# Kernel tuning notes

Measured on AMD Instinct MI355X. Metric: run time of the kernel, lower is better.

## Reference

```python
import jax, jax.numpy as jnp
import numpy as np

B, N, C = 2, 6, 64
D_BINS, D_MIN, D_MAX = 64, 1.0, 60.0
IMG_H, IMG_W = 256, 704
FH, FW = 16, 44  # image_size / 16
BEV_H, BEV_W = 200, 200
XR = (-50.0, 50.0)
YR = (-50.0, 50.0)
BN_EPS = 1e-5


def create_frustum():
    # (D, FH, FW, 3) with last dim = (x_pix, y_pix, depth)
    ds = jnp.linspace(D_MIN, D_MAX, D_BINS)
    xs = jnp.linspace(0.0, IMG_W - 1.0, FW)
    ys = jnp.linspace(0.0, IMG_H - 1.0, FH)
    d, y, x = jnp.meshgrid(ds, ys, xs, indexing='ij')
    return jnp.stack([x, y, d], axis=-1)


def _conv(x, w, b, pad):
    y = jax.lax.conv_general_dilated(x, w, (1, 1), [(pad, pad), (pad, pad)],
                                     dimension_numbers=('NCHW', 'OIHW', 'NCHW'))
    return y + b[None, :, None, None]


def setup_inputs():
    key = jax.random.key(0)
    ks = jax.random.split(key, 4)
    features = jax.random.normal(ks[0], (B, N, C, FH, FW), jnp.float32)
    # realistic pinhole intrinsics
    fx = fy = 500.0
    K = jnp.array([[fx, 0.0, IMG_W / 2.0], [0.0, fy, IMG_H / 2.0], [0.0, 0.0, 1.0]], jnp.float32)
    intrinsics = jnp.broadcast_to(K, (B, N, 3, 3)).astype(jnp.float32)
    # cam2ego: yaw rotation per camera + small translation
    yaws = jnp.arange(N, dtype=jnp.float32) * (2.0 * np.pi / N)
    def ext(yaw):
        c, s = jnp.cos(yaw), jnp.sin(yaw)
        R = jnp.array([[c, -s, 0.0], [s, c, 0.0], [0.0, 0.0, 1.0]])
        return jnp.eye(4).at[:3, :3].set(R).at[:3, 3].set(jnp.array([1.0, 0.0, 1.5]))
    extrinsics = jnp.broadcast_to(jax.vmap(ext)(yaws), (B, N, 4, 4)).astype(jnp.float32)
    # DepthNet params: conv3x3(C->C) -> BN -> ReLU -> conv1x1(C->D)
    w1 = jax.random.normal(ks[1], (C, C, 3, 3), jnp.float32) * 0.05
    b1 = jnp.zeros((C,), jnp.float32)
    gamma = jnp.ones((C,), jnp.float32)
    beta = jnp.zeros((C,), jnp.float32)
    rmean = jnp.zeros((C,), jnp.float32)
    rvar = jnp.ones((C,), jnp.float32)
    w2 = jax.random.normal(ks[2], (D_BINS, C, 1, 1), jnp.float32) * 0.05
    b2 = jnp.zeros((D_BINS,), jnp.float32)
    return dict(features=features, intrinsics=intrinsics, extrinsics=extrinsics,
                w1=w1, b1=b1, gamma=gamma, beta=beta, rmean=rmean, rvar=rvar, w2=w2, b2=b2)


def reference(features, intrinsics, extrinsics, w1, b1, gamma, beta, rmean, rvar, w2, b2):
    feat = features.reshape(B * N, C, FH, FW)
    # DepthNet (BN in eval mode with running stats)
    h = _conv(feat, w1, b1, 1)
    h = (h - rmean[None, :, None, None]) * (gamma / jnp.sqrt(rvar + BN_EPS))[None, :, None, None] \
        + beta[None, :, None, None]
    h = jax.nn.relu(h)
    depth_logits = _conv(h, w2, b2, 0)                 # (BN, D, FH, FW)
    depth_probs = jax.nn.softmax(depth_logits, axis=1)
    # lift: outer product of features and depth distribution
    vol = feat[:, :, None] * depth_probs[:, None]      # (BN, C, D, FH, FW)
    vol = vol.reshape(B, N, C, D_BINS, FH, FW)

    frustum = create_frustum()                         # (D, FH, FW, 3)
    x, y, d = frustum[..., 0], frustum[..., 1], frustum[..., 2]
    pts = jnp.stack([x * d, y * d, d], axis=0).reshape(3, -1)   # (3, P), P = D*FH*FW
    Kinv = jnp.linalg.inv(intrinsics)                  # (B, N, 3, 3)
    cam = jnp.einsum('bnij,jp->bnip', Kinv, pts)       # camera-frame points
    R, t = extrinsics[..., :3, :3], extrinsics[..., :3, 3]
    ego = jnp.einsum('bnij,bnjp->bnip', R, cam) + t[..., None]  # (B, N, 3, P)

    resx = (XR[1] - XR[0]) / BEV_W
    resy = (YR[1] - YR[0]) / BEV_H
    ix = jnp.floor((ego[:, :, 0] - XR[0]) / resx).astype(jnp.int32)  # (B, N, P)
    iy = jnp.floor((ego[:, :, 1] - YR[0]) / resy).astype(jnp.int32)
    valid = (ix >= 0) & (ix < BEV_W) & (iy >= 0) & (iy < BEV_H)
    bidx = jnp.arange(B, dtype=jnp.int32)[:, None, None]
    idx = jnp.where(valid, bidx * (BEV_H * BEV_W) + iy * BEV_W + ix, 0)

    # splat: scatter-add depth-weighted features into the BEV grid
    vol_pts = vol.reshape(B, N, C, -1) * valid[:, :, None].astype(vol.dtype)
    vals = vol_pts.transpose(0, 1, 3, 2).reshape(-1, C)  # (B*N*P, C)
    bev = jax.ops.segment_sum(vals, idx.reshape(-1), num_segments=B * BEV_H * BEV_W)
    return bev.reshape(B, BEV_H, BEV_W, C).transpose(0, 3, 1, 2)  # (B, C, bevH, bevW)
```

## Files before the change

### kernel.cpp

```cpp
#include <hip/hip_runtime.h>
#include <math.h>

#define B_   2
#define N_   6
#define C_   64
#define D_   64
#define FH_  16
#define FW_  44
#define BN_  (B_*N_)
#define PIX_ (FH_*FW_)
#define NPIX (BN_*PIX_)
#define NPTS (BN_*D_*PIX_)
#define PPBN (D_*PIX_)
#define BEVH 200
#define BEVW 200
#define NCELL (BEVH*BEVW)
#define NBCELL (B_*NCELL)
#define NSCANB ((NBCELL + 255)/256)
#define PPW  32
#define GBLK (NPTS/(PPW*4))
#define NXCD 8
#define GCHUNK (GBLK/NXCD)
#define SCBLK (NPTS/256)

#define NB_ZOUT 5000
#define NB_ZSP  313
#define NB_TW   160
#define NB_PREP 1
#define NB_FT   132
#define NB_SETUP (NB_ZOUT + NB_ZSP + NB_TW + NB_PREP + NB_FT)

__global__ __launch_bounds__(256) void setup_kernel(
        const float* __restrict__ feat, const float* __restrict__ w1,
        const float* __restrict__ w2,
        const float* __restrict__ gamma, const float* __restrict__ beta,
        const float* __restrict__ rmean, const float* __restrict__ rvar,
        const float* __restrict__ intr,
        float* __restrict__ zt, int* __restrict__ startp,
        float* __restrict__ w1t, float* __restrict__ w2t,
        float* __restrict__ bns, float* __restrict__ bnsh,
        float* __restrict__ kinv, float* __restrict__ feat_t) {
#pragma clang fp contract(off)
    __shared__ float lds[64][65];
    int blk = blockIdx.x;
    int t   = threadIdx.x;

    if (blk < NB_ZOUT) {
        ((float4*)zt)[blk*256 + t] = float4{0.f, 0.f, 0.f, 0.f};
        return;
    }
    blk -= NB_ZOUT;
    if (blk < NB_ZSP) {
        int i = blk*256 + t;
        if (i < NBCELL + 1) startp[i] = 0;
        return;
    }
    blk -= NB_ZSP;
    if (blk < NB_TW) {
        int idx = blk*256 + t;
        if (idx < C_*C_*9) {
            int cout  = idx / (C_*9);
            int r     = idx % (C_*9);
            int cin   = r / 9;
            int tap   = r % 9;
            int chunk = cin >> 4;
            int g4    = (cin & 15) >> 2;
            int l4    = cin & 3;
            w1t[((((chunk*9 + tap)*4 + g4)*64 + cout)*4) + l4] = w1[idx];
        } else if (idx < C_*C_*9 + D_*C_) {
            int j = idx - C_*C_*9;
            int d = j / C_, c = j % C_;
            w2t[c*D_ + d] = w2[j];
        }
        return;
    }
    blk -= NB_TW;
    if (blk < NB_PREP) {
        if (t < C_) {
            float s = gamma[t] / sqrtf(rvar[t] + 1e-5f);
            bns[t]  = s;
            bnsh[t] = beta[t] - rmean[t] * s;
        }
        if (t < BN_) {
            const float* K = intr + t*9;
            float A[3][3];
            for (int r = 0; r < 3; r++)
                for (int cc = 0; cc < 3; cc++) A[r][cc] = K[r*3 + cc];
            int ipiv[3];
            for (int j = 0; j < 3; j++) {
                int p = j; float mx = fabsf(A[j][j]);
                for (int i = j+1; i < 3; i++) {
                    float v = fabsf(A[i][j]);
                    if (v > mx) { mx = v; p = i; }
                }
                ipiv[j] = p;
                if (p != j)
                    for (int k = 0; k < 3; k++) { float tm = A[j][k]; A[j][k] = A[p][k]; A[p][k] = tm; }
                float rpiv = 1.0f / A[j][j];
                for (int i = j+1; i < 3; i++) A[i][j] = A[i][j] * rpiv;
                for (int k = j+1; k < 3; k++)
                    for (int i = j+1; i < 3; i++)
                        A[i][k] = A[i][k] - A[i][j] * A[j][k];
            }
            for (int j = 0; j < 3; j++) {
                float ajj = 1.0f / A[j][j];
                A[j][j] = ajj;
                float najj = -ajj;
                for (int jj = 0; jj < j; jj++) {
                    float temp = A[jj][j];
                    for (int i = 0; i < jj; i++) A[i][j] = A[i][j] + temp * A[i][jj];
                    A[jj][j] = A[jj][j] * A[jj][jj];
                }
                for (int i = 0; i < j; i++) A[i][j] = A[i][j] * najj;
            }
            for (int j = 1; j >= 0; j--) {
                float work[3];
                for (int i = j+1; i < 3; i++) { work[i] = A[i][j]; A[i][j] = 0.0f; }
                for (int k = j+1; k < 3; k++)
                    for (int i = 0; i < 3; i++)
                        A[i][j] = A[i][j] - A[i][k] * work[k];
            }
            for (int j = 2; j >= 0; j--) {
                int p = ipiv[j];
                if (p != j)
                    for (int i = 0; i < 3; i++) { float tm = A[i][j]; A[i][j] = A[i][p]; A[i][p] = tm; }
            }
            for (int k = 0; k < 9; k++) kinv[t*9 + k] = A[k/3][k%3];
        }
        return;
    }
    blk -= NB_PREP;
    {
        int bn   = blk / 11;
        int pb   = (blk % 11) * 64;
        int lane = t & 63;
        int r0   = t >> 6;
#pragma unroll
        for (int rr = 0; rr < 16; rr++) {
            int c = r0 + 4*rr;
            lds[c][lane] = feat[((size_t)bn*C_ + c)*PIX_ + pb + lane];
        }
        __syncthreads();
#pragma unroll
        for (int rr = 0; rr < 16; rr++) {
            int pr = r0 + 4*rr;
            feat_t[((size_t)bn*PIX_ + pb + pr)*C_ + lane] = lds[lane][pr];
        }
    }
}

__global__ __launch_bounds__(256) void enc_kernel(
        const float* __restrict__ feat_t,
        const float* __restrict__ w1t, const float* __restrict__ w2t,
        const float* __restrict__ bns, const float* __restrict__ bnsh,
        const float* __restrict__ b1,  const float* __restrict__ b2,
        float* __restrict__ probs) {
    __shared__ float wlds[9*C_*16];
    __shared__ float flds[36][C_];
    __shared__ float hl[16][C_];
    int blk = blockIdx.x;
    int bn  = blk / 44;
    int rem = blk % 44;
    int yt  = rem / 11;
    int xt  = rem % 11;
    int t   = threadIdx.x;
    int c   = t & 63;
    int w   = __builtin_amdgcn_readfirstlane(t >> 6);
    int y0  = yt*4;
    int x0  = xt*4;
    int y   = y0 + w;

    for (int s = w; s < 36; s += 4) {
        int srow = s / 6, scol = s % 6;
        int grow = y0 - 1 + srow;
        int gcol = x0 - 1 + scol;
        float v = 0.f;
        if (grow >= 0 && grow < FH_ && gcol >= 0 && gcol < FW_)
            v = feat_t[((size_t)bn*PIX_ + grow*FW_ + gcol)*C_ + c];
        flds[s][c] = v;
    }

    float h0 = b1[c], h1 = h0, h2 = h0, h3 = h0;

    for (int cc16 = 0; cc16 < 4; cc16++) {
        __syncthreads();
        {
            const float4* s4 = (const float4*)(w1t + cc16*(9*C_*16));
            float4* d4 = (float4*)wlds;
#pragma unroll
            for (int i = 0; i < 9; i++)
                d4[t + 256*i] = s4[t + 256*i];
        }
        __syncthreads();
        int cc = cc16*16;
#pragma unroll
        for (int g4 = 0; g4 < 4; g4++) {
            float4 wv4[9];
#pragma unroll
            for (int tap = 0; tap < 9; tap++)
                wv4[tap] = *(const float4*)&wlds[((tap*4 + g4)*64 + c)*4];
            float4 fr4[3][6];
#pragma unroll
            for (int r = 0; r < 3; r++)
#pragma unroll
                for (int cl = 0; cl < 6; cl++)
                    fr4[r][cl] = *(const float4*)&flds[(w + r)*6 + cl][cc + g4*4];
#pragma unroll
            for (int k = 0; k < 4; k++) {
#pragma unroll
                for (int ky = 0; ky < 3; ky++) {
#pragma unroll
                    for (int kx = 0; kx < 3; kx++) {
                        float wv = ((const float*)&wv4[ky*3 + kx])[k];
                        h0 = fmaf(wv, ((const float*)&fr4[ky][kx + 0])[k], h0);
                        h1 = fmaf(wv, ((const float*)&fr4[ky][kx + 1])[k], h1);
                        h2 = fmaf(wv, ((const float*)&fr4[ky][kx + 2])[k], h2);
                        h3 = fmaf(wv, ((const float*)&fr4[ky][kx + 3])[k], h3);
                    }
                }
            }
        }
    }

    float sc = bns[c], sh = bnsh[c];
    {
        float v0 = fmaf(h0, sc, sh); hl[w*4 + 0][c] = v0 > 0.f ? v0 : 0.f;
        float v1 = fmaf(h1, sc, sh); hl[w*4 + 1][c] = v1 > 0.f ? v1 : 0.f;
        float v2 = fmaf(h2, sc, sh); hl[w*4 + 2][c] = v2 > 0.f ? v2 : 0.f;
        float v3 = fmaf(h3, sc, sh); hl[w*4 + 3][c] = v3 > 0.f ? v3 : 0.f;
    }
    __syncthreads();

    float l0 = b2[c], l1 = l0, l2 = l0, l3 = l0;
    for (int c2 = 0; c2 < C_; c2++) {
        float wv = w2t[c2*D_ + c];
        l0 = fmaf(wv, hl[w*4 + 0][c2], l0);
        l1 = fmaf(wv, hl[w*4 + 1][c2], l1);
        l2 = fmaf(wv, hl[w*4 + 2][c2], l2);
        l3 = fmaf(wv, hl[w*4 + 3][c2], l3);
    }

    float lv[4] = {l0, l1, l2, l3};
#pragma unroll
    for (int p = 0; p < 4; p++) {
        float l = lv[p];
        float m = l;
        for (int off = 32; off; off >>= 1) m = fmaxf(m, __shfl_xor(m, off));
        float e = expf(l - m);
        float s = e;
        for (int off = 32; off; off >>= 1) s += __shfl_xor(s, off);
        probs[((size_t)bn*PIX_ + y*FW_ + x0 + p)*D_ + c] = e / s;
    }
}

__device__ __forceinline__ int compute_cell(int i, const float* __restrict__ kinv,
                                            const float* __restrict__ ext) {
#pragma clang fp contract(off)
    int x  = i % FW_;
    int y  = (i / FW_) % FH_;
    int d  = (i / PIX_) % D_;
    int bn = i / PPBN;

    const float* kv = kinv + bn*9;
    const float* e  = ext  + bn*16;

    float u  = (x == FW_-1) ? 703.0f : (float)((double)x * (703.0/43.0));
    float vv = (float)((double)y * 17.0);
    float dd = (d == D_-1) ? 60.0f  : (float)(1.0 + (double)d * (59.0/63.0));

    float px = u * dd;
    float py = vv * dd;
    float pz = dd;

    float cx = (kv[0]*px + kv[1]*py) + kv[2]*pz;
    float cy = (kv[3]*px + kv[4]*py) + kv[5]*pz;
    float cz = (kv[6]*px + kv[7]*py) + kv[8]*pz;

    float ex = (e[0]*cx + e[1]*cy) + e[2]*cz;
    float ey = (e[4]*cx + e[5]*cy) + e[6]*cz;
    ex = ex + e[3];
    ey = ey + e[7];

    float gx = (ex + 50.0f) / 0.5f;
    float gy = (ey + 50.0f) / 0.5f;
    int ix = (int)floorf(gx);
    int iy = (int)floorf(gy);
    return (ix >= 0 && ix < BEVW && iy >= 0 && iy < BEVH) ? (iy*BEVW + ix) : -1;
}

__device__ __forceinline__ void run_info(int fc, int lane,
                                         bool& isLeader, int& runLen, int& lead) {
    int prev = __shfl_up(fc, 1);
    isLeader = (lane == 0) || (fc != prev);
    unsigned long long mask = __ballot(isLeader);
    unsigned long long hi = (lane == 63) ? 0ull : (mask >> (lane + 1));
    int next = hi ? (lane + 1 + __builtin_ctzll(hi)) : 64;
    runLen = next - lane;
    unsigned long long lo = mask & (~0ull >> (63 - lane));
    lead = 63 - __builtin_clzll(lo);
}

__global__ __launch_bounds__(256) void geomhist_kernel(
        const float* __restrict__ ext, const float* __restrict__ kinv,
        int* __restrict__ counts) {
    int i = blockIdx.x * 256 + threadIdx.x;
    int lane = threadIdx.x & 63;
    int fc = -1;
    if (i < NPTS) {
        int cell = compute_cell(i, kinv, ext);
        if (cell >= 0) fc = (i / (PPBN * N_)) * NCELL + cell;
    }
    bool isLeader; int runLen, lead;
    run_info(fc, lane, isLeader, runLen, lead);
    if (isLeader && fc >= 0) atomicAdd(&counts[fc], runLen);
}

__global__ __launch_bounds__(256) void scanA_kernel(
        int* __restrict__ startp, int* __restrict__ cursor, int* __restrict__ bsum) {
    __shared__ int sdata[256];
    int t = threadIdx.x;
    int i = blockIdx.x * 256 + t;
    int v = (i < NBCELL) ? startp[1 + i] : 0;
    sdata[t] = v;
    __syncthreads();
#pragma unroll
    for (int off = 1; off < 256; off <<= 1) {
        int add = (t >= off) ? sdata[t - off] : 0;
        __syncthreads();
        sdata[t] += add;
        __syncthreads();
    }
    if (i < NBCELL) {
        startp[1 + i] = sdata[t];
        cursor[i]     = sdata[t] - v;
    }
    if (t == 255) bsum[blockIdx.x] = sdata[255];
}

__global__ __launch_bounds__(512) void scanC_kernel(
        int* __restrict__ startp, int* __restrict__ cursor,
        const int* __restrict__ bsum) {
    __shared__ int sdata[512];
    int t = threadIdx.x;
    int v = (t < NSCANB) ? bsum[t] : 0;
    sdata[t] = v;
    __syncthreads();
#pragma unroll
    for (int off = 1; off < 512; off <<= 1) {
        int add = (t >= off) ? sdata[t - off] : 0;
        __syncthreads();
        sdata[t] += add;
        __syncthreads();
    }
    int i = blockIdx.x * 512 + t;
    if (i >= NBCELL) return;
    int j = i >> 8;
    int off = (j == 0) ? 0 : sdata[j - 1];
    startp[1 + i] += off;
    cursor[i]     += off;
}

__global__ __launch_bounds__(256) void geomscatter_kernel(
        const float* __restrict__ ext, const float* __restrict__ kinv,
        const float* __restrict__ probs,
        int* __restrict__ cursor, int2* __restrict__ plist2) {
    int blk = (blockIdx.x % NXCD) * (SCBLK/NXCD) + blockIdx.x / NXCD;
    int i = blk * 256 + threadIdx.x;
    int lane = threadIdx.x & 63;
    int fc = -1, pixg = 0;
    float pr = 0.f;
    if (i < NPTS) {
        int cell = compute_cell(i, kinv, ext);
        if (cell >= 0) {
            int pix = i % PIX_;
            int d   = (i / PIX_) % D_;
            int bn  = i / PPBN;
            fc   = (bn / N_) * NCELL + cell;
            pixg = bn*PIX_ + pix;
            pr   = probs[(size_t)pixg*D_ + d];
        }
    }
    bool isLeader; int runLen, lead;
    run_info(fc, lane, isLeader, runLen, lead);
    int base = 0;
    if (isLeader && fc >= 0) base = atomicAdd(&cursor[fc], runLen);
    base = __shfl(base, lead);
    if (fc >= 0)
        plist2[base + (lane - lead)] = make_int2(__float_as_int(pr),
                                                 pixg | (fc << 14));
}

__device__ __forceinline__ float cell_accum(
        const int2* __restrict__ plist2, const float* __restrict__ feat_t,
        int q0, int q1, int lane) {
    float a0 = 0.f, a1 = 0.f, a2 = 0.f, a3 = 0.f;
    float a4 = 0.f, a5 = 0.f, a6 = 0.f, a7 = 0.f;
    int q = q0;
    for (; q + 8 <= q1; q += 8) {
        int2 r0 = plist2[q];
        int2 r1 = plist2[q + 1];
        int2 r2 = plist2[q + 2];
        int2 r3 = plist2[q + 3];
        int2 r4 = plist2[q + 4];
        int2 r5 = plist2[q + 5];
        int2 r6 = plist2[q + 6];
        int2 r7 = plist2[q + 7];
        float f0 = feat_t[(size_t)(r0.y & 0x3FFF)*C_ + lane];
        float f1 = feat_t[(size_t)(r1.y & 0x3FFF)*C_ + lane];
        float f2 = feat_t[(size_t)(r2.y & 0x3FFF)*C_ + lane];
        float f3 = feat_t[(size_t)(r3.y & 0x3FFF)*C_ + lane];
        float f4 = feat_t[(size_t)(r4.y & 0x3FFF)*C_ + lane];
        float f5 = feat_t[(size_t)(r5.y & 0x3FFF)*C_ + lane];
        float f6 = feat_t[(size_t)(r6.y & 0x3FFF)*C_ + lane];
        float f7 = feat_t[(size_t)(r7.y & 0x3FFF)*C_ + lane];
        a0 = fmaf(__int_as_float(r0.x), f0, a0);
        a1 = fmaf(__int_as_float(r1.x), f1, a1);
        a2 = fmaf(__int_as_float(r2.x), f2, a2);
        a3 = fmaf(__int_as_float(r3.x), f3, a3);
        a4 = fmaf(__int_as_float(r4.x), f4, a4);
        a5 = fmaf(__int_as_float(r5.x), f5, a5);
        a6 = fmaf(__int_as_float(r6.x), f6, a6);
        a7 = fmaf(__int_as_float(r7.x), f7, a7);
    }
    for (; q + 4 <= q1; q += 4) {
        int2 r0 = plist2[q];
        int2 r1 = plist2[q + 1];
        int2 r2 = plist2[q + 2];
        int2 r3 = plist2[q + 3];
        float f0 = feat_t[(size_t)(r0.y & 0x3FFF)*C_ + lane];
        float f1 = feat_t[(size_t)(r1.y & 0x3FFF)*C_ + lane];
        float f2 = feat_t[(size_t)(r2.y & 0x3FFF)*C_ + lane];
        float f3 = feat_t[(size_t)(r3.y & 0x3FFF)*C_ + lane];
        a0 = fmaf(__int_as_float(r0.x), f0, a0);
        a1 = fmaf(__int_as_float(r1.x), f1, a1);
        a2 = fmaf(__int_as_float(r2.x), f2, a2);
        a3 = fmaf(__int_as_float(r3.x), f3, a3);
    }
    for (; q < q1; q++) {
        int2 r = plist2[q];
        a0 = fmaf(__int_as_float(r.x),
                  feat_t[(size_t)(r.y & 0x3FFF)*C_ + lane], a0);
    }
    return ((a0 + a1) + (a2 + a3)) + ((a4 + a5) + (a6 + a7));
}

__global__ __launch_bounds__(256) void gather4s_kernel(
        const float* __restrict__ feat_t, const int* __restrict__ startp,
        const int2* __restrict__ plist2, float* __restrict__ out_t) {
    int blk  = (blockIdx.x % NXCD) * GCHUNK + blockIdx.x / NXCD;
    int gid  = blk * 256 + threadIdx.x;
    int W    = gid >> 6;
    int lane = gid & 63;
    int total = startp[NBCELL];
    int p0 = W * PPW;
    if (p0 >= total) return;
    int pe = min(p0 + PPW, total);
    int p  = p0;

    {
        int2 r = plist2[p0];
        int fc = ((unsigned)r.y) >> 14;
        int cs = startp[fc], ce = startp[fc + 1];
        if (cs < p0) {
            if (ce - cs > 2*PPW) {
                float acc = cell_accum(plist2, feat_t, p0, min(pe, ce), lane);
                atomicAdd(out_t + (size_t)fc*C_ + lane, acc);
            }
            p = ce;
        }
    }
    while (p < pe) {
        int2 r = plist2[p];
        int fc = ((unsigned)r.y) >> 14;
        int ce = startp[fc + 1];
        bool big = (ce - p > 2*PPW);
        int b2 = big ? min(ce, pe) : ce;
        float acc = cell_accum(plist2, feat_t, p, b2, lane);
        float* addr = out_t + (size_t)fc*C_ + lane;
        if (big) atomicAdd(addr, acc);
        else     *addr = acc;
        p = ce;
    }
}

__global__ __launch_bounds__(256) void transT_kernel(
        const float* __restrict__ out_t, float* __restrict__ out) {
    __shared__ float lds[64][65];
    int blk   = blockIdx.x;
    int b     = blk / (NCELL/64);
    int cell0 = (blk % (NCELL/64)) * 64;
    int t     = threadIdx.x;
    int lane  = t & 63;
    int r0    = t >> 6;
    size_t fcb = (size_t)b*NCELL + cell0;
#pragma unroll
    for (int k = 0; k < 16; k++) {
        int r = r0 + 4*k;
        lds[r][lane] = out_t[(fcb + r)*C_ + lane];
    }
    __syncthreads();
#pragma unroll
    for (int k = 0; k < 16; k++) {
        int ch = r0 + 4*k;
        out[((size_t)(b*C_ + ch))*NCELL + cell0 + lane] = lds[lane][ch];
    }
}

__global__ __launch_bounds__(256) void gather4d_kernel(
        const float* __restrict__ feat_t, const int* __restrict__ startp,
        const int2* __restrict__ plist2, float* __restrict__ out) {
    int blk  = (blockIdx.x % NXCD) * GCHUNK + blockIdx.x / NXCD;
    int gid  = blk * 256 + threadIdx.x;
    int W    = gid >> 6;
    int lane = gid & 63;
    int total = startp[NBCELL];
    int p0 = W * PPW;
    if (p0 >= total) return;
    int pe = min(p0 + PPW, total);
    int p  = p0;

    {
        int2 r = plist2[p0];
        int fc = ((unsigned)r.y) >> 14;
        int cs = startp[fc], ce = startp[fc + 1];
        if (cs < p0) {
            if (ce - cs > 2*PPW) {
                float acc = cell_accum(plist2, feat_t, p0, min(pe, ce), lane);
                int bb   = fc >= NCELL;
                int cell = fc - bb*NCELL;
                atomicAdd(out + ((size_t)(bb*C_ + lane))*NCELL + cell, acc);
            }
            p = ce;
        }
    }
    while (p < pe) {
        int2 r = plist2[p];
        int fc = ((unsigned)r.y) >> 14;
        int ce = startp[fc + 1];
        bool big = (ce - p > 2*PPW);
        int b2 = big ? min(ce, pe) : ce;
        float acc = cell_accum(plist2, feat_t, p, b2, lane);
        int bb   = fc >= NCELL;
        int cell = fc - bb*NCELL;
        float* addr = out + ((size_t)(bb*C_ + lane))*NCELL + cell;
        if (big) atomicAdd(addr, acc);
        else     *addr = acc;
        p = ce;
    }
}

extern "C" void kernel_launch(void* const* d_in, const int* in_sizes, int n_in,
                              void* d_out, int out_size, void* d_ws, size_t ws_size,
                              hipStream_t stream) {
    const float* feat  = (const float*)d_in[0];
    const float* intr  = (const float*)d_in[1];
    const float* ext   = (const float*)d_in[2];
    const float* w1    = (const float*)d_in[3];
    const float* b1    = (const float*)d_in[4];
    const float* gamma = (const float*)d_in[5];
    const float* beta  = (const float*)d_in[6];
    const float* rmean = (const float*)d_in[7];
    const float* rvar  = (const float*)d_in[8];
    const float* w2    = (const float*)d_in[9];
    const float* b2    = (const float*)d_in[10];
    float* out = (float*)d_out;
    (void)in_sizes; (void)n_in; (void)out_size;

    int2*  plist2 = (int2*)d_ws;
    float* w1t    = (float*)(plist2 + NPTS);
    float* w2t    = w1t + C_*C_*9;
    float* bns    = w2t + D_*C_;
    float* bnsh   = bns + C_;
    float* kinv   = bnsh + C_;
    float* probs  = kinv + BN_*9;
    float* feat_t = probs + NPTS;
    int*   startp = (int*)(feat_t + NPTS);
    int*   cursor = startp + (NBCELL + 1);
    int*   bsum   = cursor + NBCELL;
    float* out_t  = (float*)(bsum + NSCANB);
    size_t need   = (size_t)((char*)(out_t + (size_t)NBCELL*C_) - (char*)d_ws);
    bool staged   = (ws_size >= need);

    float* zt = staged ? out_t : out;

    setup_kernel<<<NB_SETUP, 256, 0, stream>>>(feat, w1, w2, gamma, beta,
                                               rmean, rvar, intr, zt, startp,
                                               w1t, w2t, bns, bnsh, kinv, feat_t);
    enc_kernel<<<528, 256, 0, stream>>>(feat_t, w1t, w2t, bns, bnsh, b1, b2, probs);
    geomhist_kernel<<<NPTS/256, 256, 0, stream>>>(ext, kinv, startp + 1);
    scanA_kernel<<<NSCANB, 256, 0, stream>>>(startp, cursor, bsum);
    scanC_kernel<<<(NBCELL + 511)/512, 512, 0, stream>>>(startp, cursor, bsum);
    geomscatter_kernel<<<SCBLK, 256, 0, stream>>>(ext, kinv, probs, cursor, plist2);
    if (staged) {
        gather4s_kernel<<<GBLK, 256, 0, stream>>>(feat_t, startp, plist2, out_t);
        transT_kernel<<<NBCELL/64, 256, 0, stream>>>(out_t, out);
    } else {
        gather4d_kernel<<<GBLK, 256, 0, stream>>>(feat_t, startp, plist2, out);
    }
}
```

Baseline: 166.7 us.

## Halve encoder conv tile to 2x4 pixels and stream weights in 8-channel chunks

The depth-net conv kernel now computes a 2x4 pixel tile per block instead of 4x4, with each wave producing 2 pixels instead of 4. Weights are staged in 8-input-channel chunks instead of 16, which shrinks LDS use and register pressure and doubles the grid to 1056 blocks. The aim is more parallelism and occupancy for a small, latency-bound kernel. The cost is twice as many weight-chunk loads and barriers per block, plus more redundant halo feature loads.

```diff
diff --git a/kernel.cpp b/kernel.cpp
--- a/kernel.cpp
+++ b/kernel.cpp
@@ -30,6 +30,8 @@
 #define NB_FT   132
 #define NB_SETUP (NB_ZOUT + NB_ZSP + NB_TW + NB_PREP + NB_FT)
 
+#define WCHUNK (9*2*C_*4)
+
 __global__ __launch_bounds__(256) void setup_kernel(
         const float* __restrict__ feat, const float* __restrict__ w1,
         const float* __restrict__ w2,
@@ -63,10 +65,10 @@
             int r     = idx % (C_*9);
             int cin   = r / 9;
             int tap   = r % 9;
-            int chunk = cin >> 4;
-            int g4    = (cin & 15) >> 2;
+            int ch8   = cin >> 3;
+            int g42   = (cin & 7) >> 2;
             int l4    = cin & 3;
-            w1t[((((chunk*9 + tap)*4 + g4)*64 + cout)*4) + l4] = w1[idx];
+            w1t[ch8*WCHUNK + (((tap*2 + g42)*64 + cout)*4) + l4] = w1[idx];
         } else if (idx < C_*C_*9 + D_*C_) {
             int j = idx - C_*C_*9;
             int d = j / C_, c = j % C_;
@@ -155,22 +157,25 @@
         const float* __restrict__ bns, const float* __restrict__ bnsh,
         const float* __restrict__ b1,  const float* __restrict__ b2,
         float* __restrict__ probs) {
-    __shared__ float wlds[9*C_*16];
-    __shared__ float flds[36][C_];
-    __shared__ float hl[16][C_];
+    __shared__ float wlds[WCHUNK];
+    __shared__ float flds[24][C_];
+    __shared__ float hl[8][C_];
     int blk = blockIdx.x;
-    int bn  = blk / 44;
-    int rem = blk % 44;
+    int bn  = blk / 88;
+    int rem = blk % 88;
     int yt  = rem / 11;
     int xt  = rem % 11;
     int t   = threadIdx.x;
     int c   = t & 63;
     int w   = __builtin_amdgcn_readfirstlane(t >> 6);
-    int y0  = yt*4;
+    int y0  = yt*2;
     int x0  = xt*4;
-    int y   = y0 + w;
-
-    for (int s = w; s < 36; s += 4) {
+    int ry  = w & 1;
+    int cg2 = w >> 1;
+    int y   = y0 + ry;
+    int xb  = x0 + cg2*2;
+
+    for (int s = w; s < 24; s += 4) {
         int srow = s / 6, scol = s % 6;
         int grow = y0 - 1 + srow;
         int gcol = x0 - 1 + scol;
@@ -180,31 +185,30 @@
         flds[s][c] = v;
     }
 
-    float h0 = b1[c], h1 = h0, h2 = h0, h3 = h0;
-
-    for (int cc16 = 0; cc16 < 4; cc16++) {
+    float h0 = b1[c], h1 = h0;
+
+    for (int ch = 0; ch < 8; ch++) {
         __syncthreads();
         {
-            const float4* s4 = (const float4*)(w1t + cc16*(9*C_*16));
+            const float4* s4 = (const float4*)(w1t + ch*WCHUNK);
             float4* d4 = (float4*)wlds;
-#pragma unroll
-            for (int i = 0; i < 9; i++)
-                d4[t + 256*i] = s4[t + 256*i];
-        }
-        __syncthreads();
-        int cc = cc16*16;
-#pragma unroll
-        for (int g4 = 0; g4 < 4; g4++) {
+            for (int i = t; i < WCHUNK/4; i += 256)
+                d4[i] = s4[i];
+        }
+        __syncthreads();
+#pragma unroll
+        for (int g42 = 0; g42 < 2; g42++) {
             float4 wv4[9];
 #pragma unroll
             for (int tap = 0; tap < 9; tap++)
-                wv4[tap] = *(const float4*)&wlds[((tap*4 + g4)*64 + c)*4];
-            float4 fr4[3][6];
+                wv4[tap] = *(const float4*)&wlds[((tap*2 + g42)*64 + c)*4];
+            int cb = ch*8 + g42*4;
+            float4 fr4[3][4];
 #pragma unroll
             for (int r = 0; r < 3; r++)
 #pragma unroll
-                for (int cl = 0; cl < 6; cl++)
-                    fr4[r][cl] = *(const float4*)&flds[(w + r)*6 + cl][cc + g4*4];
+                for (int cl = 0; cl < 4; cl++)
+                    fr4[r][cl] = *(const float4*)&flds[(ry + r)*6 + cg2*2 + cl][cb];
 #pragma unroll
             for (int k = 0; k < 4; k++) {
 #pragma unroll
@@ -214,8 +218,6 @@
                         float wv = ((const float*)&wv4[ky*3 + kx])[k];
                         h0 = fmaf(wv, ((const float*)&fr4[ky][kx + 0])[k], h0);
                         h1 = fmaf(wv, ((const float*)&fr4[ky][kx + 1])[k], h1);
-                        h2 = fmaf(wv, ((const float*)&fr4[ky][kx + 2])[k], h2);
-                        h3 = fmaf(wv, ((const float*)&fr4[ky][kx + 3])[k], h3);
                     }
                 }
             }
@@ -223,33 +225,30 @@
     }
 
     float sc = bns[c], sh = bnsh[c];
+    int slot = ry*4 + cg2*2;
     {
-        float v0 = fmaf(h0, sc, sh); hl[w*4 + 0][c] = v0 > 0.f ? v0 : 0.f;
-        float v1 = fmaf(h1, sc, sh); hl[w*4 + 1][c] = v1 > 0.f ? v1 : 0.f;
-        float v2 = fmaf(h2, sc, sh); hl[w*4 + 2][c] = v2 > 0.f ? v2 : 0.f;
-        float v3 = fmaf(h3, sc, sh); hl[w*4 + 3][c] = v3 > 0.f ? v3 : 0.f;
+        float v0 = fmaf(h0, sc, sh); hl[slot + 0][c] = v0 > 0.f ? v0 : 0.f;
+        float v1 = fmaf(h1, sc, sh); hl[slot + 1][c] = v1 > 0.f ? v1 : 0.f;
     }
     __syncthreads();
 
-    float l0 = b2[c], l1 = l0, l2 = l0, l3 = l0;
+    float l0 = b2[c], l1 = l0;
     for (int c2 = 0; c2 < C_; c2++) {
         float wv = w2t[c2*D_ + c];
-        l0 = fmaf(wv, hl[w*4 + 0][c2], l0);
-        l1 = fmaf(wv, hl[w*4 + 1][c2], l1);
-        l2 = fmaf(wv, hl[w*4 + 2][c2], l2);
-        l3 = fmaf(wv, hl[w*4 + 3][c2], l3);
-    }
-
-    float lv[4] = {l0, l1, l2, l3};
-#pragma unroll
-    for (int p = 0; p < 4; p++) {
+        l0 = fmaf(wv, hl[slot + 0][c2], l0);
+        l1 = fmaf(wv, hl[slot + 1][c2], l1);
+    }
+
+    float lv[2] = {l0, l1};
+#pragma unroll
+    for (int p = 0; p < 2; p++) {
         float l = lv[p];
         float m = l;
         for (int off = 32; off; off >>= 1) m = fmaxf(m, __shfl_xor(m, off));
         float e = expf(l - m);
         float s = e;
         for (int off = 32; off; off >>= 1) s += __shfl_xor(s, off);
-        probs[((size_t)bn*PIX_ + y*FW_ + x0 + p)*D_ + c] = e / s;
+        probs[((size_t)bn*PIX_ + y*FW_ + xb + p)*D_ + c] = e / s;
     }
 }
 
@@ -586,7 +585,7 @@
     setup_kernel<<<NB_SETUP, 256, 0, stream>>>(feat, w1, w2, gamma, beta,
                                                rmean, rvar, intr, zt, startp,
                                                w1t, w2t, bns, bnsh, kinv, feat_t);
-    enc_kernel<<<528, 256, 0, stream>>>(feat_t, w1t, w2t, bns, bnsh, b1, b2, probs);
+    enc_kernel<<<1056, 256, 0, stream>>>(feat_t, w1t, w2t, bns, bnsh, b1, b2, probs);
     geomhist_kernel<<<NPTS/256, 256, 0, stream>>>(ext, kinv, startp + 1);
     scanA_kernel<<<NSCANB, 256, 0, stream>>>(startp, cursor, bsum);
     scanC_kernel<<<(NBCELL + 511)/512, 512, 0, stream>>>(startp, cursor, bsum);
```

New measurement: 168.1 us. About the same (+0.9%).
